# Kernel tuning notes

Measured on AMD Instinct MI355X. Metric: run time of the kernel, lower is better.

The kernel has to match this reference:

```python
import jax, jax.numpy as jnp
import numpy as np

N_NODES = 50000
N_EDGES = 800000
D_IN = 128
HIDDEN = 128
N_CLASSES = 10
N_GRAPHS = 128


def setup_inputs() -> dict:
    key = jax.random.key(0)
    ks = jax.random.split(key, 16)
    x = jax.random.normal(ks[0], (N_NODES, D_IN), dtype=jnp.float32)
    edge_index = jax.random.randint(ks[1], (2, N_EDGES), 0, N_NODES, dtype=jnp.int64)
    batch = jnp.sort(jax.random.randint(ks[2], (N_NODES,), 0, N_GRAPHS, dtype=jnp.int64))

    def lin(k, fin, fout):
        return jax.random.normal(k, (fin, fout), dtype=jnp.float32) / np.sqrt(fin)

    inp = {"x": x, "edge_index": edge_index, "batch": batch}
    # SAGEConv layer 1: in=D_IN, out=HIDDEN; layers 2,3: HIDDEN->HIDDEN
    dims = [(D_IN, HIDDEN), (HIDDEN, HIDDEN), (HIDDEN, HIDDEN)]
    for i, (fin, fout) in enumerate(dims, start=1):
        inp[f"Wl{i}"] = lin(ks[2 + 2 * i], fin, fout)       # neighbor transform
        inp[f"bl{i}"] = jnp.zeros((fout,), dtype=jnp.float32)
        inp[f"Wr{i}"] = lin(ks[3 + 2 * i], fin, fout)       # root transform
    inp["W1"] = lin(ks[12], HIDDEN, HIDDEN)
    inp["b1"] = jnp.zeros((HIDDEN,), dtype=jnp.float32)
    inp["W2"] = lin(ks[13], HIDDEN, N_CLASSES)
    inp["b2"] = jnp.zeros((N_CLASSES,), dtype=jnp.float32)
    return inp


def _sage_conv(x, src, dst, Wl, bl, Wr):
    # mean-aggregate neighbor features then linear; plus root linear (PyG SAGEConv)
    msg = x[src]                                               # [E, d] gather
    agg = jax.ops.segment_sum(msg, dst, num_segments=N_NODES)  # [N, d]
    cnt = jax.ops.segment_sum(jnp.ones_like(dst, dtype=x.dtype), dst,
                              num_segments=N_NODES)
    agg = agg / jnp.maximum(cnt, 1.0)[:, None]
    return agg @ Wl + bl + x @ Wr


def reference(x, edge_index, batch, Wl1, bl1, Wr1, Wl2, bl2, Wr2,
              Wl3, bl3, Wr3, W1, b1, W2, b2):
    src, dst = edge_index[0], edge_index[1]
    h = jax.nn.relu(_sage_conv(x, src, dst, Wl1, bl1, Wr1))
    h = jax.nn.relu(_sage_conv(h, src, dst, Wl2, bl2, Wr2))
    h = jax.nn.relu(_sage_conv(h, src, dst, Wl3, bl3, Wr3))
    # global_mean_pool over graph ids
    gsum = jax.ops.segment_sum(h, batch, num_segments=N_GRAPHS)
    gcnt = jax.ops.segment_sum(jnp.ones((h.shape[0],), h.dtype), batch,
                               num_segments=N_GRAPHS)
    g = gsum / jnp.maximum(gcnt, 1.0)[:, None]                 # [G, hidden]
    g = jax.nn.relu(g @ W1 + b1)
    # dropout is identity at inference (training=False)
    logits = g @ W2 + b2
    return jax.nn.log_softmax(logits, axis=-1)
```

## Files before the change

### kernel.cpp

```cpp
#include <hip/hip_runtime.h>

#define NN 50000
#define NE 800000
#define D 128
#define NG 128
#define POOL_NODES 128
#define SCAN_NB ((NN + 1023) / 1024)

typedef __attribute__((ext_vector_type(8))) short bf16x8;
typedef __attribute__((ext_vector_type(4))) float f32x4;

static __device__ __forceinline__ ushort f2bf(float f) {
    uint x = __float_as_uint(f);
    x += 0x7fffu + ((x >> 16) & 1u);
    return (ushort)(x >> 16);
}
static __device__ __forceinline__ float bf2f(ushort u) { return __uint_as_float((uint)u << 16); }
static __device__ __forceinline__ float blo16(uint u) { return __uint_as_float(u << 16); }
static __device__ __forceinline__ float bhi16(uint u) { return __uint_as_float(u & 0xffff0000u); }

#define CASTX_NB 6250
#define CASTW_NB 192
#define COUNT_NB 3125
__global__ __launch_bounds__(256) void fusedA_kernel(
    const float* __restrict__ x, ushort* __restrict__ xb,
    const float* __restrict__ Wl1, const float* __restrict__ Wr1,
    const float* __restrict__ Wl2, const float* __restrict__ Wr2,
    const float* __restrict__ Wl3, const float* __restrict__ Wr3,
    ushort* __restrict__ wlh, ushort* __restrict__ wll,
    ushort* __restrict__ wrh, ushort* __restrict__ wrl,
    const int* __restrict__ dst, int* __restrict__ cnt) {
    const int bid = blockIdx.x;
    if (bid < CASTX_NB) {
        int i = bid * 256 + threadIdx.x;
        int n = i >> 5, g = i & 31;
        float4 v = *reinterpret_cast<const float4*>(x + (size_t)n * D + g * 4);
        ushort4 o;
        o.x = f2bf(v.x); o.y = f2bf(v.y); o.z = f2bf(v.z); o.w = f2bf(v.w);
        *reinterpret_cast<ushort4*>(xb + (size_t)n * D + g * 4) = o;
    } else if (bid < CASTX_NB + CASTW_NB) {
        int i = (bid - CASTX_NB) * 256 + threadIdx.x;
        int layer = i >> 14, j = i & 16383;
        int colg = j >> 7, k = j & 127;
        const float* Wl = (layer == 0) ? Wl1 : ((layer == 1) ? Wl2 : Wl3);
        const float* Wr = (layer == 0) ? Wr1 : ((layer == 1) ? Wr2 : Wr3);
        float vl = Wl[k * 128 + colg];
        float vr = Wr[k * 128 + colg];
        ushort hl = f2bf(vl), hr = f2bf(vr);
        wlh[i] = hl; wll[i] = f2bf(vl - bf2f(hl));
        wrh[i] = hr; wrl[i] = f2bf(vr - bf2f(hr));
    } else {
        int e = (bid - CASTX_NB - CASTW_NB) * 256 + threadIdx.x;
        if (e < NE) atomicAdd(&cnt[dst[e]], 1);
    }
}

__global__ __launch_bounds__(256) void blocksum_kernel(const int* __restrict__ cnt,
                                                       int* __restrict__ bsum, int N) {
    int base = blockIdx.x * 1024 + threadIdx.x * 4;
    int s = 0;
    if (base + 3 < N) {
        int4 v = *reinterpret_cast<const int4*>(cnt + base);
        s = v.x + v.y + v.z + v.w;
    } else {
        for (int i = 0; i < 4; ++i) if (base + i < N) s += cnt[base + i];
    }
    for (int off = 32; off > 0; off >>= 1) s += __shfl_down(s, off, 64);
    __shared__ int wsum[4];
    if ((threadIdx.x & 63) == 0) wsum[threadIdx.x >> 6] = s;
    __syncthreads();
    if (threadIdx.x == 0) bsum[blockIdx.x] = wsum[0] + wsum[1] + wsum[2] + wsum[3];
}

__global__ void scansum_kernel(int* __restrict__ bsum, int* __restrict__ rowptr, int NB, int N) {
    int t = threadIdx.x;
    int v = (t < NB) ? bsum[t] : 0;
    for (int off = 1; off < 64; off <<= 1) {
        int u = __shfl_up(v, off, 64);
        if (t >= off) v += u;
    }
    if (t < NB) bsum[t] = v;
    if (t == NB - 1) rowptr[N] = v;
}

__global__ __launch_bounds__(256) void writeptr_kernel(const int* __restrict__ cnt,
                                                       const int* __restrict__ bsum,
                                                       int* __restrict__ rowptr, int N) {
    const int b = blockIdx.x;
    const int base = b * 1024 + threadIdx.x * 4;
    int vals[4];
#pragma unroll
    for (int i = 0; i < 4; ++i) vals[i] = (base + i < N) ? cnt[base + i] : 0;
    int s = vals[0] + vals[1] + vals[2] + vals[3];

    const int lane = threadIdx.x & 63, w = threadIdx.x >> 6;
    int incl = s;
    for (int off = 1; off < 64; off <<= 1) {
        int u = __shfl_up(incl, off, 64);
        if (lane >= off) incl += u;
    }
    __shared__ int wsum[4];
    if (lane == 63) wsum[w] = incl;
    __syncthreads();
    int excl = (b == 0) ? 0 : bsum[b - 1];
    for (int i = 0; i < w; ++i) excl += wsum[i];
    excl += incl - s;

    int run = excl;
#pragma unroll
    for (int i = 0; i < 4; ++i) {
        if (base + i < N) { rowptr[base + i] = run; run += vals[i]; }
    }
}

static __device__ __forceinline__ void gemm2_body(
    char* As, int rb,
    const ushort* __restrict__ ain,
    const ushort* __restrict__ wlh, const ushort* __restrict__ wll,
    const ushort* __restrict__ wrh, const ushort* __restrict__ wrl,
    const float* __restrict__ bl,
    ushort* __restrict__ y, ushort* __restrict__ z, int N) {
    const int tid = threadIdx.x;
    const int w = tid >> 6, lane = tid & 63;
    const int row0 = rb * 128;
    const int lrow = lane & 15, lk = lane >> 4;
    const int colg = w * 16 + lrow;

    bf16x8 ylh[4], yll[4], zrh[4], zrl[4];
#pragma unroll
    for (int kb = 0; kb < 4; ++kb) {
        int off = colg * 128 + kb * 32 + lk * 8;
        ylh[kb] = *reinterpret_cast<const bf16x8*>(wlh + off);
        yll[kb] = *reinterpret_cast<const bf16x8*>(wll + off);
        zrh[kb] = *reinterpret_cast<const bf16x8*>(wrh + off);
        zrl[kb] = *reinterpret_cast<const bf16x8*>(wrl + off);
    }
    const float bias = bl[colg];

    {
        const char* gbase = (const char*)ain + (size_t)row0 * 256;
#pragma unroll
        for (int i = 0; i < 4; ++i) {
            int Ld = i * 8192 + w * 1024 + lane * 16;
            int gs = Ld ^ (((Ld >> 8) & 7) << 4);
            __builtin_amdgcn_global_load_lds(
                (const uint*)(gbase + gs),
                (uint*)(As + i * 8192 + w * 1024), 16, 0, 0);
        }
    }
    __syncthreads();

#pragma unroll
    for (int mt = 0; mt < 8; ++mt) {
        const int ar = mt * 16 + lrow;
        const int swz = (ar & 7) << 4;
        const char* ap = As + ar * 256;
        bf16x8 ah[4];
#pragma unroll
        for (int kb = 0; kb < 4; ++kb) {
            int b_ = kb * 64 + lk * 16;
            ah[kb] = *reinterpret_cast<const bf16x8*>(ap + (b_ ^ swz));
        }
        f32x4 accy = {0.f, 0.f, 0.f, 0.f}, accz = {0.f, 0.f, 0.f, 0.f};
#pragma unroll
        for (int kb = 0; kb < 4; ++kb) {
            accy = __builtin_amdgcn_mfma_f32_16x16x32_bf16(ah[kb], ylh[kb], accy, 0, 0, 0);
            accy = __builtin_amdgcn_mfma_f32_16x16x32_bf16(ah[kb], yll[kb], accy, 0, 0, 0);
            accz = __builtin_amdgcn_mfma_f32_16x16x32_bf16(ah[kb], zrh[kb], accz, 0, 0, 0);
            accz = __builtin_amdgcn_mfma_f32_16x16x32_bf16(ah[kb], zrl[kb], accz, 0, 0, 0);
        }
#pragma unroll
        for (int r = 0; r < 4; ++r) {
            int rowg = row0 + mt * 16 + lk * 4 + r;
            if (rowg < N) {
                y[(size_t)rowg * D + colg] = f2bf(accy[r]);
                z[(size_t)rowg * D + colg] = f2bf(accz[r] + bias);
            }
        }
    }
}

__global__ __launch_bounds__(512, 4) void gemm2_kernel(
    const ushort* __restrict__ ain,
    const ushort* __restrict__ wlh, const ushort* __restrict__ wll,
    const ushort* __restrict__ wrh, const ushort* __restrict__ wrl,
    const float* __restrict__ bl,
    ushort* __restrict__ y, ushort* __restrict__ z, int N) {
    __shared__ char As[128 * 256];
    gemm2_body(As, blockIdx.x, ain, wlh, wll, wrh, wrl, bl, y, z, N);
}

#define GEMM_NB 391
__global__ __launch_bounds__(512, 4) void fusedB_kernel(
    const ushort* __restrict__ ain,
    const ushort* __restrict__ wlh, const ushort* __restrict__ wll,
    const ushort* __restrict__ wrh, const ushort* __restrict__ wrl,
    const float* __restrict__ bl,
    ushort* __restrict__ y, ushort* __restrict__ z,
    const int* __restrict__ src, const int* __restrict__ dst,
    const int* __restrict__ rowptr, int* __restrict__ fillp,
    int* __restrict__ col, int N) {
    __shared__ char As[128 * 256];
    const int bid = blockIdx.x;
    if (bid < GEMM_NB) {
        gemm2_body(As, bid, ain, wlh, wll, wrh, wrl, bl, y, z, N);
    } else {
        int e = (bid - GEMM_NB) * 512 + threadIdx.x;
        const int q = NE >> 2;
        if (e >= q) return;
        int d0 = dst[e];
        int d1 = dst[e + q];
        int d2 = dst[e + 2 * q];
        int d3 = dst[e + 3 * q];
        int s0 = src[e];
        int s1 = src[e + q];
        int s2 = src[e + 2 * q];
        int s3 = src[e + 3 * q];
        int p0 = atomicAdd(&fillp[d0], 1);
        int p1 = atomicAdd(&fillp[d1], 1);
        int p2 = atomicAdd(&fillp[d2], 1);
        int p3 = atomicAdd(&fillp[d3], 1);
        __hip_atomic_store(&col[rowptr[d0] + p0], s0, __ATOMIC_RELAXED, __HIP_MEMORY_SCOPE_AGENT);
        __hip_atomic_store(&col[rowptr[d1] + p1], s1, __ATOMIC_RELAXED, __HIP_MEMORY_SCOPE_AGENT);
        __hip_atomic_store(&col[rowptr[d2] + p2], s2, __ATOMIC_RELAXED, __HIP_MEMORY_SCOPE_AGENT);
        __hip_atomic_store(&col[rowptr[d3] + p3], s3, __ATOMIC_RELAXED, __HIP_MEMORY_SCOPE_AGENT);
    }
}

__global__ __launch_bounds__(256) void gather_relu(
    const ushort* __restrict__ y, ushort* __restrict__ z,
    const int* __restrict__ rowptr, const int* __restrict__ col, int N) {
    int wid = (blockIdx.x * 256 + threadIdx.x) >> 6;
    if (wid >= N) return;
    const int lane = threadIdx.x & 63;
    const int h = lane >> 5, li = lane & 31;
    int lo = rowptr[wid], hi = rowptr[wid + 1];
    float a0 = 0.f, a1 = 0.f, a2 = 0.f, a3 = 0.f;
    int e = lo + h;
    for (; e + 2 < hi; e += 4) {
        int s0 = col[e], s1 = col[e + 2];
        uint2 v0 = *reinterpret_cast<const uint2*>(y + (size_t)s0 * D + li * 4);
        uint2 v1 = *reinterpret_cast<const uint2*>(y + (size_t)s1 * D + li * 4);
        a0 += blo16(v0.x) + blo16(v1.x);
        a1 += bhi16(v0.x) + bhi16(v1.x);
        a2 += blo16(v0.y) + blo16(v1.y);
        a3 += bhi16(v0.y) + bhi16(v1.y);
    }
    for (; e < hi; e += 2) {
        uint2 v = *reinterpret_cast<const uint2*>(y + (size_t)col[e] * D + li * 4);
        a0 += blo16(v.x); a1 += bhi16(v.x);
        a2 += blo16(v.y); a3 += bhi16(v.y);
    }
    a0 += __shfl_xor(a0, 32, 64);
    a1 += __shfl_xor(a1, 32, 64);
    a2 += __shfl_xor(a2, 32, 64);
    a3 += __shfl_xor(a3, 32, 64);
    if (h == 0) {
        float inv = 1.0f / fmaxf((float)(hi - lo), 1.0f);
        uint2 zv = *reinterpret_cast<const uint2*>(z + (size_t)wid * D + li * 4);
        float h0 = fmaxf(a0 * inv + blo16(zv.x), 0.f);
        float h1 = fmaxf(a1 * inv + bhi16(zv.x), 0.f);
        float h2 = fmaxf(a2 * inv + blo16(zv.y), 0.f);
        float h3 = fmaxf(a3 * inv + bhi16(zv.y), 0.f);
        uint2 o;
        o.x = (uint)f2bf(h0) | ((uint)f2bf(h1) << 16);
        o.y = (uint)f2bf(h2) | ((uint)f2bf(h3) << 16);
        *reinterpret_cast<uint2*>(z + (size_t)wid * D + li * 4) = o;
    }
}

__global__ __launch_bounds__(256) void pool_i(
    const ushort* __restrict__ hbuf, const int* __restrict__ batch,
    float* __restrict__ gsum, int N) {
    const int lane = threadIdx.x & 63;
    const int wv = threadIdx.x >> 6;
    const int cb = lane * 2;
    const int n0 = blockIdx.x * POOL_NODES;
    const int n1 = min(n0 + POOL_NODES, N);
    int gid = -1;
    float a0 = 0.f, a1 = 0.f;
    for (int n = n0 + wv; n < n1; n += 4) {
        int b = batch[n];
        if (b != gid) {
            if (gid >= 0) {
                atomicAdd(&gsum[gid * D + cb], a0);
                atomicAdd(&gsum[gid * D + cb + 1], a1);
            }
            gid = b; a0 = a1 = 0.f;
        }
        uint v = *reinterpret_cast<const uint*>(hbuf + (size_t)n * D + cb);
        a0 += blo16(v); a1 += bhi16(v);
    }
    if (gid >= 0) {
        atomicAdd(&gsum[gid * D + cb], a0);
        atomicAdd(&gsum[gid * D + cb + 1], a1);
    }
}

__global__ __launch_bounds__(128) void head_kernel(
    const float* __restrict__ gsum, const int* __restrict__ batch, int N,
    const float* __restrict__ W1, const float* __restrict__ b1,
    const float* __restrict__ W2, const float* __restrict__ b2,
    float* __restrict__ out) {
    __shared__ float gl[128];
    __shared__ float tl[128];
    __shared__ float lg[10];
    __shared__ float red[2];
    const int b = blockIdx.x, j = threadIdx.x;

    int lo = 0, r = N;
    while (lo < r) { int m = (lo + r) >> 1; if (batch[m] < b) lo = m + 1; else r = m; }
    int hi = lo; r = N;
    while (hi < r) { int m = (hi + r) >> 1; if (batch[m] < b + 1) hi = m + 1; else r = m; }

    float c = fmaxf((float)(hi - lo), 1.0f);
    gl[j] = gsum[b * D + j] / c;
    __syncthreads();

    float t = b1[j];
    for (int k = 0; k < 128; ++k) t += gl[k] * W1[k * 128 + j];
    tl[j] = fmaxf(t, 0.0f);
    __syncthreads();

    if (j < 10) {
        float acc = b2[j];
        for (int k = 0; k < 128; ++k) acc += tl[k] * W2[k * 10 + j];
        lg[j] = acc;
    }
    __syncthreads();

    if (j == 0) {
        float m = lg[0];
        for (int q = 1; q < 10; ++q) m = fmaxf(m, lg[q]);
        float s = 0.0f;
        for (int q = 0; q < 10; ++q) s += expf(lg[q] - m);
        red[0] = m;
        red[1] = logf(s);
    }
    __syncthreads();

    if (j < 10) out[b * 10 + j] = lg[j] - red[0] - red[1];
}

extern "C" void kernel_launch(void* const* d_in, const int* in_sizes, int n_in,
                              void* d_out, int out_size, void* d_ws, size_t ws_size,
                              hipStream_t stream) {
    const float* x    = (const float*)d_in[0];
    const int*   ei   = (const int*)d_in[1];
    const int*   src  = ei;
    const int*   dst  = ei + NE;
    const int*   batch = (const int*)d_in[2];
    const float* Wl1 = (const float*)d_in[3];
    const float* bl1 = (const float*)d_in[4];
    const float* Wr1 = (const float*)d_in[5];
    const float* Wl2 = (const float*)d_in[6];
    const float* bl2 = (const float*)d_in[7];
    const float* Wr2 = (const float*)d_in[8];
    const float* Wl3 = (const float*)d_in[9];
    const float* bl3 = (const float*)d_in[10];
    const float* Wr3 = (const float*)d_in[11];
    const float* W1  = (const float*)d_in[12];
    const float* b1  = (const float*)d_in[13];
    const float* W2  = (const float*)d_in[14];
    const float* b2  = (const float*)d_in[15];
    float* out = (float*)d_out;

    char* p = (char*)d_ws;
    char* S0 = p; p += 12800000;
    char* S1 = p; p += 12800000;
    char* S2 = p; p += 12800000;
    ushort* wlh = (ushort*)p; p += 3 * 32768;
    ushort* wll = (ushort*)p; p += 3 * 32768;
    ushort* wrh = (ushort*)p; p += 3 * 32768;
    ushort* wrl = (ushort*)p; p += 3 * 32768;
    float* gsum = (float*)p; p += 65536;
    int* cnt    = (int*)p;   p += 200000;
    int* fillp  = (int*)p;   p += 200000;
    int* rowptr = (int*)p;   p += 200016;
    int* colb   = (int*)p;   p += 3200000;
    int* bsum   = (int*)p;   p += 256;

    hipMemsetAsync(cnt, 0, (size_t)NN * 4, stream);
    hipMemsetAsync(fillp, 0, (size_t)NN * 4, stream);
    hipMemsetAsync(gsum, 0, (size_t)NG * D * 4, stream);

    fusedA_kernel<<<CASTX_NB + CASTW_NB + COUNT_NB, 256, 0, stream>>>(
        x, (ushort*)S0, Wl1, Wr1, Wl2, Wr2, Wl3, Wr3, wlh, wll, wrh, wrl, dst, cnt);

    blocksum_kernel<<<SCAN_NB, 256, 0, stream>>>(cnt, bsum, NN);
    scansum_kernel<<<1, 64, 0, stream>>>(bsum, rowptr, SCAN_NB, NN);
    writeptr_kernel<<<SCAN_NB, 256, 0, stream>>>(cnt, bsum, rowptr, NN);

    const int agg_blocks = (NN * 64 + 255) / 256;

    fusedB_kernel<<<GEMM_NB + 391, 512, 0, stream>>>(
        (ushort*)S0, wlh, wll, wrh, wrl, bl1, (ushort*)S1, (ushort*)S2,
        src, dst, rowptr, fillp, colb, NN);

    gather_relu<<<agg_blocks, 256, 0, stream>>>((ushort*)S1, (ushort*)S2, rowptr, colb, NN);
    gemm2_kernel<<<GEMM_NB, 512, 0, stream>>>((ushort*)S2, wlh + 16384, wll + 16384,
                                              wrh + 16384, wrl + 16384, bl2,
                                              (ushort*)S1, (ushort*)S0, NN);
    gather_relu<<<agg_blocks, 256, 0, stream>>>((ushort*)S1, (ushort*)S0, rowptr, colb, NN);
    gemm2_kernel<<<GEMM_NB, 512, 0, stream>>>((ushort*)S0, wlh + 32768, wll + 32768,
                                              wrh + 32768, wrl + 32768, bl3,
                                              (ushort*)S1, (ushort*)S2, NN);
    gather_relu<<<agg_blocks, 256, 0, stream>>>((ushort*)S1, (ushort*)S2, rowptr, colb, NN);

    pool_i<<<(NN + POOL_NODES - 1) / POOL_NODES, 256, 0, stream>>>((ushort*)S2, batch, gsum, NN);
    head_kernel<<<NG, 128, 0, stream>>>(gsum, batch, NN, W1, b1, W2, b2, out);
}
```

Before: 291.2 us.

## Partition CSR fill by XCD dst range and split gather columns across XCDs

The CSR column fill now runs first in the fused kernel. Each block scans a slice of edges and handles only destinations in one of eight node groups, chosen by blockIdx&7, so the atomics and col writes for a range stay on one XCD's L2. Each block now reads every edge in its slice, which multiplies dst reads by eight. The gather kernel splits each node's 128 features into two 64-column halves handled by different XCD groups, so each XCD's L2 caches only half of each source row. This narrows each load from 8 to 4 bytes and doubles the number of blocks.

```diff
diff --git a/kernel.cpp b/kernel.cpp
--- a/kernel.cpp
+++ b/kernel.cpp
@@ -6,6 +6,10 @@
 #define NG 128
 #define POOL_NODES 128
 #define SCAN_NB ((NN + 1023) / 1024)
+#define NGRP 8
+#define GRPSZ 6250
+#define FILL_NB 392
+#define ESL ((NE + 48) / 49)
 
 typedef __attribute__((ext_vector_type(8))) short bf16x8;
 typedef __attribute__((ext_vector_type(4))) float f32x4;
@@ -202,70 +206,59 @@
     int* __restrict__ col, int N) {
     __shared__ char As[128 * 256];
     const int bid = blockIdx.x;
-    if (bid < GEMM_NB) {
-        gemm2_body(As, bid, ain, wlh, wll, wrh, wrl, bl, y, z, N);
+    if (bid < FILL_NB) {
+        const int grp = bid & 7;
+        const int slice = bid >> 3;
+        const int dlo = grp * GRPSZ, dhi = dlo + GRPSZ;
+        const int e0 = slice * ESL;
+        const int e1 = min(e0 + ESL, NE);
+        for (int e = e0 + (int)threadIdx.x; e < e1; e += 512) {
+            int d = dst[e];
+            if (d >= dlo && d < dhi) {
+                int s = src[e];
+                int pos = atomicAdd(&fillp[d], 1);
+                col[rowptr[d] + pos] = s;
+            }
+        }
     } else {
-        int e = (bid - GEMM_NB) * 512 + threadIdx.x;
-        const int q = NE >> 2;
-        if (e >= q) return;
-        int d0 = dst[e];
-        int d1 = dst[e + q];
-        int d2 = dst[e + 2 * q];
-        int d3 = dst[e + 3 * q];
-        int s0 = src[e];
-        int s1 = src[e + q];
-        int s2 = src[e + 2 * q];
-        int s3 = src[e + 3 * q];
-        int p0 = atomicAdd(&fillp[d0], 1);
-        int p1 = atomicAdd(&fillp[d1], 1);
-        int p2 = atomicAdd(&fillp[d2], 1);
-        int p3 = atomicAdd(&fillp[d3], 1);
-        __hip_atomic_store(&col[rowptr[d0] + p0], s0, __ATOMIC_RELAXED, __HIP_MEMORY_SCOPE_AGENT);
-        __hip_atomic_store(&col[rowptr[d1] + p1], s1, __ATOMIC_RELAXED, __HIP_MEMORY_SCOPE_AGENT);
-        __hip_atomic_store(&col[rowptr[d2] + p2], s2, __ATOMIC_RELAXED, __HIP_MEMORY_SCOPE_AGENT);
-        __hip_atomic_store(&col[rowptr[d3] + p3], s3, __ATOMIC_RELAXED, __HIP_MEMORY_SCOPE_AGENT);
+        gemm2_body(As, bid - FILL_NB, ain, wlh, wll, wrh, wrl, bl, y, z, N);
     }
 }
 
 __global__ __launch_bounds__(256) void gather_relu(
     const ushort* __restrict__ y, ushort* __restrict__ z,
     const int* __restrict__ rowptr, const int* __restrict__ col, int N) {
-    int wid = (blockIdx.x * 256 + threadIdx.x) >> 6;
-    if (wid >= N) return;
+    const int bid = blockIdx.x;
+    const int xcd = bid & 7;
+    const int half = xcd >> 2;
+    const int node = (bid >> 3) * 16 + (xcd & 3) * 4 + (int)(threadIdx.x >> 6);
+    if (node >= N) return;
     const int lane = threadIdx.x & 63;
     const int h = lane >> 5, li = lane & 31;
-    int lo = rowptr[wid], hi = rowptr[wid + 1];
-    float a0 = 0.f, a1 = 0.f, a2 = 0.f, a3 = 0.f;
+    const int cb = half * 64 + li * 2;
+    int lo = rowptr[node], hi = rowptr[node + 1];
+    float a0 = 0.f, a1 = 0.f;
     int e = lo + h;
     for (; e + 2 < hi; e += 4) {
         int s0 = col[e], s1 = col[e + 2];
-        uint2 v0 = *reinterpret_cast<const uint2*>(y + (size_t)s0 * D + li * 4);
-        uint2 v1 = *reinterpret_cast<const uint2*>(y + (size_t)s1 * D + li * 4);
-        a0 += blo16(v0.x) + blo16(v1.x);
-        a1 += bhi16(v0.x) + bhi16(v1.x);
-        a2 += blo16(v0.y) + blo16(v1.y);
-        a3 += bhi16(v0.y) + bhi16(v1.y);
+        uint v0 = *reinterpret_cast<const uint*>(y + (size_t)s0 * D + cb);
+        uint v1 = *reinterpret_cast<const uint*>(y + (size_t)s1 * D + cb);
+        a0 += blo16(v0) + blo16(v1);
+        a1 += bhi16(v0) + bhi16(v1);
     }
     for (; e < hi; e += 2) {
-        uint2 v = *reinterpret_cast<const uint2*>(y + (size_t)col[e] * D + li * 4);
-        a0 += blo16(v.x); a1 += bhi16(v.x);
-        a2 += blo16(v.y); a3 += bhi16(v.y);
+        uint v = *reinterpret_cast<const uint*>(y + (size_t)col[e] * D + cb);
+        a0 += blo16(v); a1 += bhi16(v);
     }
     a0 += __shfl_xor(a0, 32, 64);
     a1 += __shfl_xor(a1, 32, 64);
-    a2 += __shfl_xor(a2, 32, 64);
-    a3 += __shfl_xor(a3, 32, 64);
     if (h == 0) {
         float inv = 1.0f / fmaxf((float)(hi - lo), 1.0f);
-        uint2 zv = *reinterpret_cast<const uint2*>(z + (size_t)wid * D + li * 4);
-        float h0 = fmaxf(a0 * inv + blo16(zv.x), 0.f);
-        float h1 = fmaxf(a1 * inv + bhi16(zv.x), 0.f);
-        float h2 = fmaxf(a2 * inv + blo16(zv.y), 0.f);
-        float h3 = fmaxf(a3 * inv + bhi16(zv.y), 0.f);
-        uint2 o;
-        o.x = (uint)f2bf(h0) | ((uint)f2bf(h1) << 16);
-        o.y = (uint)f2bf(h2) | ((uint)f2bf(h3) << 16);
-        *reinterpret_cast<uint2*>(z + (size_t)wid * D + li * 4) = o;
+        uint zv = *reinterpret_cast<const uint*>(z + (size_t)node * D + cb);
+        float h0 = fmaxf(a0 * inv + blo16(zv), 0.f);
+        float h1 = fmaxf(a1 * inv + bhi16(zv), 0.f);
+        uint o = (uint)f2bf(h0) | ((uint)f2bf(h1) << 16);
+        *reinterpret_cast<uint*>(z + (size_t)node * D + cb) = o;
     }
 }
 
@@ -391,9 +384,9 @@
     scansum_kernel<<<1, 64, 0, stream>>>(bsum, rowptr, SCAN_NB, NN);
     writeptr_kernel<<<SCAN_NB, 256, 0, stream>>>(cnt, bsum, rowptr, NN);
 
-    const int agg_blocks = (NN * 64 + 255) / 256;
-
-    fusedB_kernel<<<GEMM_NB + 391, 512, 0, stream>>>(
+    const int agg_blocks = ((NN + 15) / 16) * 8;
+
+    fusedB_kernel<<<FILL_NB + GEMM_NB, 512, 0, stream>>>(
         (ushort*)S0, wlh, wll, wrh, wrl, bl1, (ushort*)S1, (ushort*)S2,
         src, dst, rowptr, fillp, colb, NN);
 
```

Result: slower. 341.4 us (+17.2%).

## Partition CSR fill by destination group per XCD and schedule fill blocks first

Applied to the files above, without the earlier changes.

Replaces the flat 4-edges-per-thread CSR fill with blocks organized as 8 destination groups by 49 edge slices. Each block scans its slice and only handles edges whose destination lies in its group, keeping atomic counters and column writes localized per group, likely per XCD L2. Fill blocks are placed before GEMM blocks in the fused launch. The cost is reading the dst array eight times.

```diff
diff --git a/kernel.cpp b/kernel.cpp
--- a/kernel.cpp
+++ b/kernel.cpp
@@ -6,6 +6,10 @@
 #define NG 128
 #define POOL_NODES 128
 #define SCAN_NB ((NN + 1023) / 1024)
+#define NGRP 8
+#define GRPSZ 6250
+#define FILL_NB 392
+#define ESL ((NE + 48) / 49)
 
 typedef __attribute__((ext_vector_type(8))) short bf16x8;
 typedef __attribute__((ext_vector_type(4))) float f32x4;
@@ -202,28 +206,22 @@
     int* __restrict__ col, int N) {
     __shared__ char As[128 * 256];
     const int bid = blockIdx.x;
-    if (bid < GEMM_NB) {
-        gemm2_body(As, bid, ain, wlh, wll, wrh, wrl, bl, y, z, N);
+    if (bid < FILL_NB) {
+        const int grp = bid & 7;
+        const int slice = bid >> 3;
+        const int dlo = grp * GRPSZ, dhi = dlo + GRPSZ;
+        const int e0 = slice * ESL;
+        const int e1 = min(e0 + ESL, NE);
+        for (int e = e0 + (int)threadIdx.x; e < e1; e += 512) {
+            int d = dst[e];
+            if (d >= dlo && d < dhi) {
+                int s = src[e];
+                int pos = atomicAdd(&fillp[d], 1);
+                col[rowptr[d] + pos] = s;
+            }
+        }
     } else {
-        int e = (bid - GEMM_NB) * 512 + threadIdx.x;
-        const int q = NE >> 2;
-        if (e >= q) return;
-        int d0 = dst[e];
-        int d1 = dst[e + q];
-        int d2 = dst[e + 2 * q];
-        int d3 = dst[e + 3 * q];
-        int s0 = src[e];
-        int s1 = src[e + q];
-        int s2 = src[e + 2 * q];
-        int s3 = src[e + 3 * q];
-        int p0 = atomicAdd(&fillp[d0], 1);
-        int p1 = atomicAdd(&fillp[d1], 1);
-        int p2 = atomicAdd(&fillp[d2], 1);
-        int p3 = atomicAdd(&fillp[d3], 1);
-        __hip_atomic_store(&col[rowptr[d0] + p0], s0, __ATOMIC_RELAXED, __HIP_MEMORY_SCOPE_AGENT);
-        __hip_atomic_store(&col[rowptr[d1] + p1], s1, __ATOMIC_RELAXED, __HIP_MEMORY_SCOPE_AGENT);
-        __hip_atomic_store(&col[rowptr[d2] + p2], s2, __ATOMIC_RELAXED, __HIP_MEMORY_SCOPE_AGENT);
-        __hip_atomic_store(&col[rowptr[d3] + p3], s3, __ATOMIC_RELAXED, __HIP_MEMORY_SCOPE_AGENT);
+        gemm2_body(As, bid - FILL_NB, ain, wlh, wll, wrh, wrl, bl, y, z, N);
     }
 }
 
@@ -393,7 +391,7 @@
 
     const int agg_blocks = (NN * 64 + 255) / 256;
 
-    fusedB_kernel<<<GEMM_NB + 391, 512, 0, stream>>>(
+    fusedB_kernel<<<FILL_NB + GEMM_NB, 512, 0, stream>>>(
         (ushort*)S0, wlh, wll, wrh, wrl, bl1, (ushort*)S1, (ushort*)S2,
         src, dst, rowptr, fillp, colb, NN);
 
```

New measurement: 280.3 us. 1.04x faster.
